# Optimization experiments

Measured on AMD Instinct MI355X. Metric: run time of the kernel, lower is better.

## Reference

```python
import jax, jax.numpy as jnp
import numpy as np

NUM_HEADS = 16
ROPE_THETA = 10000.0


def _rope_cos_sin(T, head_dim, dtype):
    # inv_freq over even indices; cos/sin shape [T, head_dim//2]
    inv_freq = 1.0 / (ROPE_THETA ** (jnp.arange(0, head_dim, 2, dtype=jnp.float32) / head_dim))
    t = jnp.arange(T, dtype=jnp.float32)
    freqs = jnp.outer(t, inv_freq)  # [T, hd/2]
    return jnp.cos(freqs).astype(dtype), jnp.sin(freqs).astype(dtype)


def _apply_rope(x, cos, sin):
    # x: [B,H,T,hd]; de-interleave even/odd, rotate, concat halves
    x1 = x[..., ::2]
    x2 = x[..., 1::2]
    return jnp.concatenate([x1 * cos - x2 * sin, x1 * sin + x2 * cos], axis=-1)


def setup_inputs() -> dict:
    key = jax.random.key(0)
    k1, k2, k3 = jax.random.split(key, 3)
    B, T, C = 2, 2048, 2048
    x = jax.random.normal(k1, (B, T, C), dtype=jnp.float32)
    w_qkv = jax.random.normal(k2, (3 * C, C), dtype=jnp.float32) * (C ** -0.5)
    w_proj = jax.random.normal(k3, (C, C), dtype=jnp.float32) * (C ** -0.5)
    causal_mask = jnp.tril(jnp.ones((T, T), dtype=bool))[None, None, :, :]  # [1,1,T,T]
    return {"x": x, "w_qkv": w_qkv, "w_proj": w_proj, "causal_mask": causal_mask}


def reference(x, w_qkv, w_proj, causal_mask):
    B, T, C = x.shape
    H = NUM_HEADS
    hd = C // H
    scale = hd ** -0.5

    qkv = jnp.einsum('btc,oc->bto', x, w_qkv)  # [B,T,3C]
    qkv = qkv.reshape(B, T, 3, H, hd).transpose(2, 0, 3, 1, 4)  # [3,B,H,T,hd]
    q, k, v = qkv[0], qkv[1], qkv[2]

    cos, sin = _rope_cos_sin(T, hd, x.dtype)
    q = _apply_rope(q, cos, sin)
    k = _apply_rope(k, cos, sin)

    scores = jnp.einsum('bhqd,bhkd->bhqk', q, k) * scale  # [B,H,T,T]
    scores = jnp.where(causal_mask, scores, -jnp.inf)
    attn = jax.nn.softmax(scores, axis=-1)
    out = jnp.einsum('bhqk,bhkd->bhqd', attn, v)  # [B,H,T,hd]
    out = out.transpose(0, 2, 1, 3).reshape(B, T, C)
    return jnp.einsum('btc,oc->bto', out, w_proj)
```

## Files before the change

kernel.cpp:

```cpp
#include <hip/hip_runtime.h>
#include <stdint.h>

typedef float f32x4 __attribute__((ext_vector_type(4)));
typedef __bf16 bf16x8 __attribute__((ext_vector_type(8)));
typedef unsigned short u16x8 __attribute__((ext_vector_type(8)));

__device__ __forceinline__ unsigned short f2bf(float f) {
  union { float f; unsigned u; } x; x.f = f;
  unsigned r = x.u + 0x7fffu + ((x.u >> 16) & 1u);
  return (unsigned short)(r >> 16);
}
__device__ __forceinline__ float bf2f(unsigned short u) {
  union { unsigned u; float f; } x; x.u = ((unsigned)u) << 16;
  return x.f;
}
__device__ __forceinline__ void async_copy16(void* lds, const void* g) {
  __builtin_amdgcn_global_load_lds(
      (const unsigned int __attribute__((address_space(1)))*)g,
      (unsigned int __attribute__((address_space(3)))*)lds, 16, 0, 0);
}
__device__ __forceinline__ f32x4 mfma16(bf16x8 a, bf16x8 b, f32x4 c) {
  return __builtin_amdgcn_mfma_f32_16x16x32_bf16(a, b, c, 0, 0, 0);
}

__global__ __launch_bounds__(256) void cvt_f32_bf16(
    const float* __restrict__ in, unsigned short* __restrict__ out, int n8) {
  int stride = gridDim.x * blockDim.x;
  for (int i = blockIdx.x * blockDim.x + threadIdx.x; i < n8; i += stride) {
    const float4* p = (const float4*)in + (size_t)i * 2;
    float4 a = p[0], b = p[1];
    u16x8 o;
    o[0] = f2bf(a.x); o[1] = f2bf(a.y); o[2] = f2bf(a.z); o[3] = f2bf(a.w);
    o[4] = f2bf(b.x); o[5] = f2bf(b.y); o[6] = f2bf(b.z); o[7] = f2bf(b.w);
    *((u16x8*)out + i) = o;
  }
}

__global__ __launch_bounds__(256) void rope_table(float2* __restrict__ cs) {
  int idx = blockIdx.x * 256 + threadIdx.x;
  if (idx >= 2048 * 64) return;
  int t = idx >> 6, j = idx & 63;
  float inv = expf(-0.14391156516026f * (float)j);
  float ang = (float)t * inv;
  cs[idx] = make_float2(cosf(ang), sinf(ang));
}

#define BM 128
#define BN 128
#define BK 32

template <bool OUT_F32>
__global__ __launch_bounds__(256, 2) void gemm_bt(
    const unsigned short* __restrict__ A, const unsigned short* __restrict__ Bt,
    void* __restrict__ Cout, int M, int N, int K) {
  __shared__ unsigned short sA[2][BM * BK];
  __shared__ unsigned short sB[2][BN * BK];
  const int tid = threadIdx.x;
  const int w = tid >> 6, l = tid & 63;
  const int m0 = blockIdx.y * BM, n0 = blockIdx.x * BN;
  const int wr = w >> 1, wc = w & 1;
  const int g = l >> 4, lr = l & 15;

  f32x4 acc[4][4];
#pragma unroll
  for (int i = 0; i < 4; ++i)
#pragma unroll
    for (int j = 0; j < 4; ++j) acc[i][j] = f32x4{0.f, 0.f, 0.f, 0.f};

  const int rl = l >> 2, ps = l & 3;
  auto stage = [&](int buf, int k0) {
#pragma unroll
    for (int i = 0; i < 2; ++i) {
      int region = w + i * 4;
      int row = region * 16 + rl;
      int s = ps ^ (row & 3);
      async_copy16(&sA[buf][region * 16 * BK],
                   A + (size_t)(m0 + row) * K + k0 + s * 8);
      async_copy16(&sB[buf][region * 16 * BK],
                   Bt + (size_t)(n0 + row) * K + k0 + s * 8);
    }
  };

  stage(0, 0);
  int cur = 0;
  const int NK = K / BK;
  for (int kt = 0; kt < NK; ++kt) {
    asm volatile("s_waitcnt vmcnt(0)" ::: "memory");
    __syncthreads();
    if (kt + 1 < NK) stage(cur ^ 1, (kt + 1) * BK);

    bf16x8 af[4], bfr[4];
#pragma unroll
    for (int mi = 0; mi < 4; ++mi) {
      int row = wr * 64 + mi * 16 + lr;
      af[mi] = *(const bf16x8*)&sA[cur][row * BK + ((g ^ (row & 3)) << 3)];
    }
#pragma unroll
    for (int ni = 0; ni < 4; ++ni) {
      int row = wc * 64 + ni * 16 + lr;
      bfr[ni] = *(const bf16x8*)&sB[cur][row * BK + ((g ^ (row & 3)) << 3)];
    }
#pragma unroll
    for (int mi = 0; mi < 4; ++mi)
#pragma unroll
      for (int ni = 0; ni < 4; ++ni)
        acc[mi][ni] = mfma16(af[mi], bfr[ni], acc[mi][ni]);
    __syncthreads();
    cur ^= 1;
  }

#pragma unroll
  for (int mi = 0; mi < 4; ++mi)
#pragma unroll
    for (int ni = 0; ni < 4; ++ni) {
      int col = n0 + wc * 64 + ni * 16 + lr;
#pragma unroll
      for (int jr = 0; jr < 4; ++jr) {
        int row = m0 + wr * 64 + mi * 16 + g * 4 + jr;
        float v = acc[mi][ni][jr];
        if (OUT_F32)
          ((float*)Cout)[(size_t)row * N + col] = v;
        else
          ((unsigned short*)Cout)[(size_t)row * N + col] = f2bf(v);
      }
    }
}

__global__ __launch_bounds__(256) void prep_rope(
    const unsigned short* __restrict__ qkv, const float2* __restrict__ cs,
    unsigned short* __restrict__ Q, unsigned short* __restrict__ K,
    unsigned short* __restrict__ Vt) {
  const int tt = blockIdx.x, h = blockIdx.y, b = blockIdx.z;
  const int t0 = tt * 64;
  const int tid = threadIdx.x;
  __shared__ unsigned short vt[64][130];

#pragma unroll 4
  for (int i = 0; i < 32; ++i) {
    int lin = i * 256 + tid;
    int r = lin >> 7, j = lin & 127;
    int t = t0 + r;
    int jj = j & 63;
    size_t rowbase = ((size_t)(b * 2048 + t)) * 6144 + h * 128;
    float2 c_s = cs[t * 64 + jj];
    float q1 = bf2f(qkv[rowbase + 2 * jj]);
    float q2 = bf2f(qkv[rowbase + 2 * jj + 1]);
    float k1 = bf2f(qkv[rowbase + 2048 + 2 * jj]);
    float k2 = bf2f(qkv[rowbase + 2048 + 2 * jj + 1]);
    float qo = (j < 64) ? (q1 * c_s.x - q2 * c_s.y) : (q1 * c_s.y + q2 * c_s.x);
    float ko = (j < 64) ? (k1 * c_s.x - k2 * c_s.y) : (k1 * c_s.y + k2 * c_s.x);
    size_t obase = ((size_t)((b * 16 + h) * 2048 + t)) * 128 + j;
    Q[obase] = f2bf(qo);
    K[obase] = f2bf(ko);
    vt[r][j] = qkv[rowbase + 4096 + j];
  }
  __syncthreads();
  size_t vbase = ((size_t)((b * 16 + h) * 128)) * 2048 + t0;
#pragma unroll 4
  for (int i = 0; i < 32; ++i) {
    int lin = i * 256 + tid;
    int d = lin >> 6, c = lin & 63;
    Vt[vbase + (size_t)d * 2048 + c] = vt[c][d];
  }
}

__global__ __launch_bounds__(512, 2) void attn_fwd(
    const unsigned short* __restrict__ Q, const unsigned short* __restrict__ K,
    const unsigned short* __restrict__ Vt, unsigned short* __restrict__ AO) {
  const int bid = blockIdx.x;
  const int bh = (bid & 7) * 4 + ((bid >> 3) & 3);
  const int qp = bid >> 5;
  const int b = bh >> 4, h = bh & 15;
  __shared__ unsigned short sK[2][64 * 128];
  __shared__ unsigned short sV[2][128 * 64];
  __shared__ unsigned short sP[8][16 * 64];
  const int tid = threadIdx.x, w = tid >> 6, l = tid & 63;
  const int g = l >> 4, lr = l & 15;
  const size_t qkbase = (size_t)bh * 2048 * 128;
  const size_t vbase = (size_t)bh * 128 * 2048;
  const float scale = 0.08838834764831845f;

  auto stage = [&](int buf, int kt) {
#pragma unroll
    for (int j = 0; j < 2; ++j) {
      int r = w * 2 + j;
      int kv = r * 4 + (l >> 4);
      int sc = (l & 15) ^ (kv & 15);
      async_copy16(&sK[buf][r * 512],
                   K + qkbase + (size_t)(kt * 64 + kv) * 128 + sc * 8);
      int d = r * 8 + (l >> 3);
      int sv = (l & 7) ^ (d & 7);
      async_copy16(&sV[buf][r * 512],
                   Vt + vbase + (size_t)d * 2048 + kt * 64 + sv * 8);
    }
  };

  auto process = [&](int qt) {
    const int q0w = qt * 128 + w * 16;
    bf16x8 qf[4];
#pragma unroll
    for (int kc = 0; kc < 4; ++kc)
      qf[kc] = *(const bf16x8*)(Q + qkbase + (size_t)(q0w + lr) * 128 +
                                kc * 32 + g * 8);
    f32x4 of[8];
    float mrow[4], lsum[4];
#pragma unroll
    for (int nd = 0; nd < 8; ++nd) of[nd] = f32x4{0.f, 0.f, 0.f, 0.f};
#pragma unroll
    for (int jr = 0; jr < 4; ++jr) { mrow[jr] = -1e30f; lsum[jr] = 0.f; }

    const int NT = 2 * qt + 2;
    __syncthreads();
    stage(0, 0);
    int cur = 0;
    for (int kt = 0; kt < NT; ++kt) {
      asm volatile("s_waitcnt vmcnt(0)" ::: "memory");
      __syncthreads();
      if (kt + 1 < NT) stage(cur ^ 1, kt + 1);

      if (kt * 64 <= q0w + 15) {
        f32x4 sacc[4];
#pragma unroll
        for (int ni = 0; ni < 4; ++ni) sacc[ni] = f32x4{0.f, 0.f, 0.f, 0.f};
#pragma unroll
        for (int kc = 0; kc < 4; ++kc)
#pragma unroll
          for (int ni = 0; ni < 4; ++ni) {
            int kv = ni * 16 + lr;
            bf16x8 kf = *(const bf16x8*)&sK[cur][kv * 128 +
                          (((kc * 4 + g) ^ (kv & 15)) << 3)];
            sacc[ni] = mfma16(qf[kc], kf, sacc[ni]);
          }

        const bool needmask = (kt * 64 + 63 > q0w);
        float pm[4] = {-1e30f, -1e30f, -1e30f, -1e30f};
#pragma unroll
        for (int ni = 0; ni < 4; ++ni)
#pragma unroll
          for (int jr = 0; jr < 4; ++jr) {
            float sv = sacc[ni][jr] * scale;
            if (needmask) {
              int kvg = kt * 64 + ni * 16 + lr;
              int qg = q0w + g * 4 + jr;
              if (kvg > qg) sv = -1e30f;
            }
            sacc[ni][jr] = sv;
            pm[jr] = fmaxf(pm[jr], sv);
          }
#pragma unroll
        for (int jr = 0; jr < 4; ++jr) {
          float v = pm[jr];
          v = fmaxf(v, __shfl_xor(v, 1));
          v = fmaxf(v, __shfl_xor(v, 2));
          v = fmaxf(v, __shfl_xor(v, 4));
          v = fmaxf(v, __shfl_xor(v, 8));
          float mnew = fmaxf(mrow[jr], v);
          float fac = __expf(mrow[jr] - mnew);
          mrow[jr] = mnew;
          float rsum = 0.f;
#pragma unroll
          for (int ni = 0; ni < 4; ++ni) {
            float p = __expf(sacc[ni][jr] - mnew);
            sacc[ni][jr] = p;
            rsum += p;
          }
          rsum += __shfl_xor(rsum, 1);
          rsum += __shfl_xor(rsum, 2);
          rsum += __shfl_xor(rsum, 4);
          rsum += __shfl_xor(rsum, 8);
          lsum[jr] = lsum[jr] * fac + rsum;
#pragma unroll
          for (int nd = 0; nd < 8; ++nd) of[nd][jr] *= fac;
        }

#pragma unroll
        for (int ni = 0; ni < 4; ++ni)
#pragma unroll
          for (int jr = 0; jr < 4; ++jr) {
            int q = g * 4 + jr;
            int kv = ni * 16 + lr;
            sP[w][q * 64 + (((kv >> 3) ^ (q & 7)) << 3) + (kv & 7)] =
                f2bf(sacc[ni][jr]);
          }

#pragma unroll
        for (int kc = 0; kc < 2; ++kc) {
          bf16x8 pa = *(const bf16x8*)&sP[w][lr * 64 +
                        (((kc * 4 + g) ^ (lr & 7)) << 3)];
#pragma unroll
          for (int nd = 0; nd < 8; ++nd) {
            int d = nd * 16 + lr;
            bf16x8 vb = *(const bf16x8*)&sV[cur][d * 64 +
                          (((kc * 4 + g) ^ (d & 7)) << 3)];
            of[nd] = mfma16(pa, vb, of[nd]);
          }
        }
      }
      cur ^= 1;
    }

#pragma unroll
    for (int nd = 0; nd < 8; ++nd)
#pragma unroll
      for (int jr = 0; jr < 4; ++jr) {
        int qrow = q0w + g * 4 + jr;
        int d = nd * 16 + lr;
        AO[(size_t)(b * 2048 + qrow) * 2048 + h * 128 + d] =
            f2bf(of[nd][jr] / lsum[jr]);
      }
  };

  process(qp);
  process(15 - qp);
}

extern "C" void kernel_launch(void* const* d_in, const int* in_sizes, int n_in,
                              void* d_out, int out_size, void* d_ws, size_t ws_size,
                              hipStream_t stream) {
  (void)in_sizes; (void)n_in; (void)out_size; (void)ws_size;
  const float* x = (const float*)d_in[0];
  const float* wqkv = (const float*)d_in[1];
  const float* wproj = (const float*)d_in[2];

  char* ws = (char*)d_ws;
  unsigned short* WPROJB = (unsigned short*)(ws + 0);
  unsigned short* XB     = (unsigned short*)(ws + 8388608);
  unsigned short* WQKVB  = (unsigned short*)(ws + 25165824);
  unsigned short* QKV    = (unsigned short*)(ws + 50331648);
  unsigned short* Kr     = (unsigned short*)(ws + 100663296);
  unsigned short* Vt     = (unsigned short*)(ws + 117440512);
  float2*         CS     = (float2*)(ws + 134217728);
  unsigned short* AO = XB;
  unsigned short* Qr = WQKVB;

  rope_table<<<512, 256, 0, stream>>>(CS);
  cvt_f32_bf16<<<2048, 256, 0, stream>>>(x, XB, 8388608 / 8);
  cvt_f32_bf16<<<2048, 256, 0, stream>>>(wqkv, WQKVB, 12582912 / 8);
  cvt_f32_bf16<<<1024, 256, 0, stream>>>(wproj, WPROJB, 4194304 / 8);
  gemm_bt<false><<<dim3(48, 32), 256, 0, stream>>>(XB, WQKVB, QKV, 4096, 6144, 2048);
  prep_rope<<<dim3(32, 16, 2), 256, 0, stream>>>(QKV, CS, Qr, Kr, Vt);
  attn_fwd<<<256, 512, 0, stream>>>(Qr, Kr, Vt, AO);
  gemm_bt<true><<<dim3(16, 32), 256, 0, stream>>>(AO, WPROJB, d_out, 4096, 2048, 2048);
}
```

Baseline: 447.0 us.

## Use 128x256 GEMM tiles with 8 waves and triple-buffered async loads

```diff
diff --git a/kernel.cpp b/kernel.cpp
--- a/kernel.cpp
+++ b/kernel.cpp
@@ -45,21 +45,17 @@
   cs[idx] = make_float2(cosf(ang), sinf(ang));
 }
 
-#define BM 128
-#define BN 128
-#define BK 32
-
 template <bool OUT_F32>
-__global__ __launch_bounds__(256, 2) void gemm_bt(
+__global__ __launch_bounds__(512, 2) void gemm_bt2(
     const unsigned short* __restrict__ A, const unsigned short* __restrict__ Bt,
     void* __restrict__ Cout, int M, int N, int K) {
-  __shared__ unsigned short sA[2][BM * BK];
-  __shared__ unsigned short sB[2][BN * BK];
+  __shared__ unsigned short sA[3][128 * 32];
+  __shared__ unsigned short sB[3][256 * 32];
   const int tid = threadIdx.x;
   const int w = tid >> 6, l = tid & 63;
-  const int m0 = blockIdx.y * BM, n0 = blockIdx.x * BN;
-  const int wr = w >> 1, wc = w & 1;
+  const int wm = w >> 2, wn = w & 3;
   const int g = l >> 4, lr = l & 15;
+  const int m0 = blockIdx.y * 128, n0 = blockIdx.x * 256;
 
   f32x4 acc[4][4];
 #pragma unroll
@@ -67,56 +63,66 @@
 #pragma unroll
     for (int j = 0; j < 4; ++j) acc[i][j] = f32x4{0.f, 0.f, 0.f, 0.f};
 
-  const int rl = l >> 2, ps = l & 3;
-  auto stage = [&](int buf, int k0) {
-#pragma unroll
-    for (int i = 0; i < 2; ++i) {
-      int region = w + i * 4;
-      int row = region * 16 + rl;
-      int s = ps ^ (row & 3);
-      async_copy16(&sA[buf][region * 16 * BK],
-                   A + (size_t)(m0 + row) * K + k0 + s * 8);
-      async_copy16(&sB[buf][region * 16 * BK],
-                   Bt + (size_t)(n0 + row) * K + k0 + s * 8);
+  auto stage = [&](int buf, int kt) {
+    const int k0 = kt * 32;
+    {
+      int unit = w * 64 + l;
+      int row = unit >> 2, s = unit & 3;
+      int sg = s ^ (row & 3) ^ ((row >> 2) & 3);
+      async_copy16(&sA[buf][w * 512],
+                   A + (size_t)(m0 + row) * K + k0 + sg * 8);
+    }
+#pragma unroll
+    for (int j = 0; j < 2; ++j) {
+      int unit = j * 512 + w * 64 + l;
+      int row = unit >> 2, s = unit & 3;
+      int sg = s ^ (row & 3) ^ ((row >> 2) & 3);
+      async_copy16(&sB[buf][(j * 8 + w) * 512],
+                   Bt + (size_t)(n0 + row) * K + k0 + sg * 8);
     }
   };
 
+  const int NK = K / 32;
   stage(0, 0);
-  int cur = 0;
-  const int NK = K / BK;
+  stage(1, 1);
   for (int kt = 0; kt < NK; ++kt) {
-    asm volatile("s_waitcnt vmcnt(0)" ::: "memory");
+    const int cur = kt % 3;
+    if (kt + 1 < NK) asm volatile("s_waitcnt vmcnt(3)" ::: "memory");
+    else             asm volatile("s_waitcnt vmcnt(0)" ::: "memory");
     __syncthreads();
-    if (kt + 1 < NK) stage(cur ^ 1, (kt + 1) * BK);
-
-    bf16x8 af[4], bfr[4];
+    if (kt + 2 < NK) stage((kt + 2) % 3, kt + 2);
+
+    bf16x8 af[4], bq[4];
 #pragma unroll
     for (int mi = 0; mi < 4; ++mi) {
-      int row = wr * 64 + mi * 16 + lr;
-      af[mi] = *(const bf16x8*)&sA[cur][row * BK + ((g ^ (row & 3)) << 3)];
+      int row = wm * 64 + mi * 16 + lr;
+      int sl = g ^ (row & 3) ^ ((row >> 2) & 3);
+      af[mi] = *(const bf16x8*)&sA[cur][row * 32 + sl * 8];
     }
 #pragma unroll
     for (int ni = 0; ni < 4; ++ni) {
-      int row = wc * 64 + ni * 16 + lr;
-      bfr[ni] = *(const bf16x8*)&sB[cur][row * BK + ((g ^ (row & 3)) << 3)];
-    }
+      int row = wn * 64 + ni * 16 + lr;
+      int sl = g ^ (row & 3) ^ ((row >> 2) & 3);
+      bq[ni] = *(const bf16x8*)&sB[cur][row * 32 + sl * 8];
+    }
+    __builtin_amdgcn_s_setprio(1);
 #pragma unroll
     for (int mi = 0; mi < 4; ++mi)
 #pragma unroll
       for (int ni = 0; ni < 4; ++ni)
-        acc[mi][ni] = mfma16(af[mi], bfr[ni], acc[mi][ni]);
+        acc[mi][ni] = mfma16(af[mi], bq[ni], acc[mi][ni]);
+    __builtin_amdgcn_s_setprio(0);
     __syncthreads();
-    cur ^= 1;
   }
 
 #pragma unroll
   for (int mi = 0; mi < 4; ++mi)
 #pragma unroll
     for (int ni = 0; ni < 4; ++ni) {
-      int col = n0 + wc * 64 + ni * 16 + lr;
+      int col = n0 + wn * 64 + ni * 16 + lr;
 #pragma unroll
       for (int jr = 0; jr < 4; ++jr) {
-        int row = m0 + wr * 64 + mi * 16 + g * 4 + jr;
+        int row = m0 + wm * 64 + mi * 16 + g * 4 + jr;
         float v = acc[mi][ni][jr];
         if (OUT_F32)
           ((float*)Cout)[(size_t)row * N + col] = v;
@@ -337,8 +343,8 @@
   cvt_f32_bf16<<<2048, 256, 0, stream>>>(x, XB, 8388608 / 8);
   cvt_f32_bf16<<<2048, 256, 0, stream>>>(wqkv, WQKVB, 12582912 / 8);
   cvt_f32_bf16<<<1024, 256, 0, stream>>>(wproj, WPROJB, 4194304 / 8);
-  gemm_bt<false><<<dim3(48, 32), 256, 0, stream>>>(XB, WQKVB, QKV, 4096, 6144, 2048);
+  gemm_bt2<false><<<dim3(24, 32), 512, 0, stream>>>(XB, WQKVB, QKV, 4096, 6144, 2048);
   prep_rope<<<dim3(32, 16, 2), 256, 0, stream>>>(QKV, CS, Qr, Kr, Vt);
   attn_fwd<<<256, 512, 0, stream>>>(Qr, Kr, Vt, AO);
-  gemm_bt<true><<<dim3(16, 32), 256, 0, stream>>>(AO, WPROJB, d_out, 4096, 2048, 2048);
-}
+  gemm_bt2<true><<<dim3(8, 32), 512, 0, stream>>>(AO, WPROJB, d_out, 4096, 2048, 2048);
+}
```

Result: slower. 464.2 us (+3.8%).
